# Optimization experiments

Hardware: AMD Instinct MI355X
Metric: run time of the kernel (lower is better)

The kernel has to match this reference:

```python
import jax, jax.numpy as jnp
import numpy as np


def setup_inputs() -> dict:
    key = jax.random.key(0)
    k1, k2 = jax.random.split(key)
    pred_corners = jax.random.normal(k1, (2048, 8, 3), dtype=jnp.float32)
    gt_corners = jax.random.normal(k2, (2048, 8, 3), dtype=jnp.float32)
    return {"pred_corners": pred_corners, "gt_corners": gt_corners}


def _chamfer(pred_corners, gt_corners):
    # flatten boxes -> point clouds: [Np*8, 3], [Ng*8, 3]
    x = pred_corners.reshape(-1, 3)
    y = gt_corners.reshape(-1, 3)
    x2 = jnp.sum(x * x, axis=-1)  # [N]
    y2 = jnp.sum(y * y, axis=-1)  # [M]
    d2 = x2[:, None] + y2[None, :] - 2.0 * jnp.einsum("nd,md->nm", x, y)
    dist = jnp.sqrt(jnp.maximum(d2, 0.0))  # [N, M]
    # bidirectional min, averaged per box (8 corners) then over boxes
    min_p2g = jnp.min(dist, axis=1).reshape(-1, 8).mean(axis=1)
    min_g2p = jnp.min(dist, axis=0).reshape(-1, 8).mean(axis=1)
    return min_p2g.mean() + min_g2p.mean()


def reference(pred_corners, gt_corners):
    return _chamfer(pred_corners, gt_corners)
```

## Files before the change

### kernel.cpp

```cpp
#include <hip/hip_runtime.h>


#define NPTS   16384
#define RPT    16
#define BLOCK  256
#define XPB    (RPT * BLOCK)
#define NXB    (NPTS / XPB)
#define NSEG   128
#define YSEG   (NPTS / NSEG)

__global__ __launch_bounds__(256) void init_mins(unsigned int* mins) {
    int i = blockIdx.x * blockDim.x + threadIdx.x;
    if (i < 2 * NPTS) mins[i] = 0x7F800000u;
}

__global__ __launch_bounds__(BLOCK, 4) void chamfer_min(
        const float* __restrict__ pred, const float* __restrict__ gt,
        unsigned int* __restrict__ mins) {
    const int xb  = blockIdx.x;
    const int ys  = blockIdx.y;
    const int dir = blockIdx.z;
    const float* __restrict__ X = dir ? gt : pred;
    const float* __restrict__ Y = dir ? pred : gt;
    unsigned int* __restrict__ outm = mins + dir * NPTS;
    const int tid = threadIdx.x;

    __shared__ float4 sh[YSEG];

    if (tid < YSEG) {
        int yi = ys * YSEG + tid;
        float a = Y[3 * yi + 0], b = Y[3 * yi + 1], c = Y[3 * yi + 2];
        sh[tid] = make_float4(a, b, c, -0.5f * (a * a + b * b + c * c));
    }

    float xx[RPT], xy[RPT], xz[RPT], x2[RPT], mx[RPT];
    const int xbase = xb * XPB;
#pragma unroll
    for (int r = 0; r < RPT; ++r) {
        int xi = xbase + r * BLOCK + tid;
        xx[r] = X[3 * xi + 0];
        xy[r] = X[3 * xi + 1];
        xz[r] = X[3 * xi + 2];
        x2[r] = xx[r] * xx[r] + xy[r] * xy[r] + xz[r] * xz[r];
        mx[r] = -3.0e38f;
    }

    __syncthreads();

#pragma unroll 2
    for (int j = 0; j < YSEG; ++j) {
        float4 y = sh[j];
#pragma unroll
        for (int r = 0; r < RPT; ++r) {
            float t = fmaf(xz[r], y.z, y.w);
            t = fmaf(xy[r], y.y, t);
            t = fmaf(xx[r], y.x, t);
            mx[r] = fmaxf(mx[r], t);
        }
    }

#pragma unroll
    for (int r = 0; r < RPT; ++r) {
        int xi = xbase + r * BLOCK + tid;
        float d2 = fmaxf(fmaf(-2.0f, mx[r], x2[r]), 0.0f);
        atomicMin(&outm[xi], __float_as_uint(d2));
    }
}

__global__ __launch_bounds__(1024) void chamfer_reduce(
        const unsigned int* __restrict__ mins, float* __restrict__ out) {
    const int tid = threadIdx.x;
    float s = 0.0f;
    for (int i = tid; i < 2 * NPTS; i += 1024)
        s += sqrtf(__uint_as_float(mins[i]));

#pragma unroll
    for (int off = 32; off > 0; off >>= 1)
        s += __shfl_down(s, off, 64);

    __shared__ float part[16];
    if ((tid & 63) == 0) part[tid >> 6] = s;
    __syncthreads();
    if (tid == 0) {
        float t = 0.0f;
#pragma unroll
        for (int w = 0; w < 16; ++w) t += part[w];
        out[0] = t / (float)NPTS;
    }
}

extern "C" void kernel_launch(void* const* d_in, const int* in_sizes, int n_in,
                              void* d_out, int out_size, void* d_ws, size_t ws_size,
                              hipStream_t stream) {
    const float* pred = (const float*)d_in[0];
    const float* gt   = (const float*)d_in[1];
    float* out        = (float*)d_out;
    unsigned int* mins = (unsigned int*)d_ws;

    hipLaunchKernelGGL(init_mins, dim3((2 * NPTS + 255) / 256), dim3(256), 0, stream,
                       mins);
    hipLaunchKernelGGL(chamfer_min, dim3(NXB, NSEG, 2), dim3(BLOCK), 0, stream,
                       pred, gt, mins);
    hipLaunchKernelGGL(chamfer_reduce, dim3(1), dim3(1024), 0, stream, mins, out);
}
```

Measured before the change: 107.2 us.

## Replace atomicMin with per-segment partial buffer and multi-block combine reduction

When the workspace is large enough, the main kernel writes each Y-segment's per-point max to a partial buffer instead of issuing atomicMin. A separate combine kernel takes the min over 64 segments, applies the sqrt and reduces per block, and a small final kernel sums the block results. This removes atomic contention and the single-block reduction, at the cost of an 8 MB partial buffer written and read back. Tile sizes also change (RPT 8, NSEG 64), the inner loop is unrolled by two Y points, and the fallback atomic path gets a multi-block reduction that uses atomicAdd.

```diff
diff --git a/kernel.cpp b/kernel.cpp
--- a/kernel.cpp
+++ b/kernel.cpp
@@ -2,19 +2,114 @@
 
 
 #define NPTS   16384
-#define RPT    16
+#define RPT    8
 #define BLOCK  256
 #define XPB    (RPT * BLOCK)
 #define NXB    (NPTS / XPB)
-#define NSEG   128
+#define NSEG   64
 #define YSEG   (NPTS / NSEG)
-
-__global__ __launch_bounds__(256) void init_mins(unsigned int* mins) {
+#define NPART  (2 * NSEG * NPTS)
+#define K2B    128
+#define WS_NEED ((NPART + K2B) * 4)
+
+
+__global__ __launch_bounds__(BLOCK, 4) void chamfer_partial(
+        const float* __restrict__ pred, const float* __restrict__ gt,
+        float* __restrict__ part) {
+    const int xb  = blockIdx.x;
+    const int ys  = blockIdx.y;
+    const int dir = blockIdx.z;
+    const float* __restrict__ X = dir ? gt : pred;
+    const float* __restrict__ Y = dir ? pred : gt;
+    const int tid = threadIdx.x;
+
+    __shared__ float4 sh[YSEG];
+    {
+        int yi = ys * YSEG + tid;
+        float a = Y[3 * yi + 0], b = Y[3 * yi + 1], c = Y[3 * yi + 2];
+        sh[tid] = make_float4(a, b, c, -0.5f * (a * a + b * b + c * c));
+    }
+
+    float xx[RPT], xy[RPT], xz[RPT], x2[RPT], mx[RPT];
+    const int xbase = xb * XPB;
+#pragma unroll
+    for (int r = 0; r < RPT; ++r) {
+        int xi = xbase + r * BLOCK + tid;
+        xx[r] = X[3 * xi + 0];
+        xy[r] = X[3 * xi + 1];
+        xz[r] = X[3 * xi + 2];
+        x2[r] = xx[r] * xx[r] + xy[r] * xy[r] + xz[r] * xz[r];
+        mx[r] = -3.0e38f;
+    }
+
+    __syncthreads();
+
+#pragma unroll 2
+    for (int j = 0; j < YSEG; j += 2) {
+        float4 y0 = sh[j];
+        float4 y1 = sh[j + 1];
+#pragma unroll
+        for (int r = 0; r < RPT; ++r) {
+            float t0 = fmaf(xz[r], y0.z, y0.w);
+            t0 = fmaf(xy[r], y0.y, t0);
+            t0 = fmaf(xx[r], y0.x, t0);
+            float t1 = fmaf(xz[r], y1.z, y1.w);
+            t1 = fmaf(xy[r], y1.y, t1);
+            t1 = fmaf(xx[r], y1.x, t1);
+            mx[r] = fmaxf(mx[r], fmaxf(t0, t1));
+        }
+    }
+
+    float* __restrict__ dst = part + (dir * NSEG + ys) * NPTS;
+#pragma unroll
+    for (int r = 0; r < RPT; ++r) {
+        int xi = xbase + r * BLOCK + tid;
+        dst[xi] = fmaf(-2.0f, mx[r], x2[r]);
+    }
+}
+
+__global__ __launch_bounds__(256) void chamfer_combine(
+        const float* __restrict__ part, float* __restrict__ sums) {
+    const int gid = blockIdx.x * 256 + threadIdx.x;
+    const int dir = gid >> 14;
+    const int x   = gid & (NPTS - 1);
+    float m = 3.0e38f;
+#pragma unroll 8
+    for (int s = 0; s < NSEG; ++s)
+        m = fminf(m, part[(dir * NSEG + s) * NPTS + x]);
+    float v = sqrtf(fmaxf(m, 0.0f));
+
+#pragma unroll
+    for (int off = 32; off > 0; off >>= 1)
+        v += __shfl_down(v, off, 64);
+
+    __shared__ float lsum[4];
+    if ((threadIdx.x & 63) == 0) lsum[threadIdx.x >> 6] = v;
+    __syncthreads();
+    if (threadIdx.x == 0)
+        sums[blockIdx.x] = lsum[0] + lsum[1] + lsum[2] + lsum[3];
+}
+
+__global__ __launch_bounds__(128) void chamfer_final(
+        const float* __restrict__ sums, float* __restrict__ out) {
+    float v = sums[threadIdx.x];
+#pragma unroll
+    for (int off = 32; off > 0; off >>= 1)
+        v += __shfl_down(v, off, 64);
+    __shared__ float w[2];
+    if ((threadIdx.x & 63) == 0) w[threadIdx.x >> 6] = v;
+    __syncthreads();
+    if (threadIdx.x == 0) out[0] = (w[0] + w[1]) * (1.0f / (float)NPTS);
+}
+
+
+__global__ __launch_bounds__(256) void init_mins(unsigned int* mins, float* out) {
     int i = blockIdx.x * blockDim.x + threadIdx.x;
     if (i < 2 * NPTS) mins[i] = 0x7F800000u;
-}
-
-__global__ __launch_bounds__(BLOCK, 4) void chamfer_min(
+    if (i == 0) out[0] = 0.0f;
+}
+
+__global__ __launch_bounds__(BLOCK, 4) void chamfer_min_atomic(
         const float* __restrict__ pred, const float* __restrict__ gt,
         unsigned int* __restrict__ mins) {
     const int xb  = blockIdx.x;
@@ -26,13 +121,11 @@
     const int tid = threadIdx.x;
 
     __shared__ float4 sh[YSEG];
-
-    if (tid < YSEG) {
+    {
         int yi = ys * YSEG + tid;
         float a = Y[3 * yi + 0], b = Y[3 * yi + 1], c = Y[3 * yi + 2];
         sh[tid] = make_float4(a, b, c, -0.5f * (a * a + b * b + c * c));
     }
-
     float xx[RPT], xy[RPT], xz[RPT], x2[RPT], mx[RPT];
     const int xbase = xb * XPB;
 #pragma unroll
@@ -44,21 +137,21 @@
         x2[r] = xx[r] * xx[r] + xy[r] * xy[r] + xz[r] * xz[r];
         mx[r] = -3.0e38f;
     }
-
-    __syncthreads();
-
+    __syncthreads();
 #pragma unroll 2
-    for (int j = 0; j < YSEG; ++j) {
-        float4 y = sh[j];
+    for (int j = 0; j < YSEG; j += 2) {
+        float4 y0 = sh[j], y1 = sh[j + 1];
 #pragma unroll
         for (int r = 0; r < RPT; ++r) {
-            float t = fmaf(xz[r], y.z, y.w);
-            t = fmaf(xy[r], y.y, t);
-            t = fmaf(xx[r], y.x, t);
-            mx[r] = fmaxf(mx[r], t);
+            float t0 = fmaf(xz[r], y0.z, y0.w);
+            t0 = fmaf(xy[r], y0.y, t0);
+            t0 = fmaf(xx[r], y0.x, t0);
+            float t1 = fmaf(xz[r], y1.z, y1.w);
+            t1 = fmaf(xy[r], y1.y, t1);
+            t1 = fmaf(xx[r], y1.x, t1);
+            mx[r] = fmaxf(mx[r], fmaxf(t0, t1));
         }
     }
-
 #pragma unroll
     for (int r = 0; r < RPT; ++r) {
         int xi = xbase + r * BLOCK + tid;
@@ -67,26 +160,18 @@
     }
 }
 
-__global__ __launch_bounds__(1024) void chamfer_reduce(
+__global__ __launch_bounds__(256) void chamfer_reduce_atomic(
         const unsigned int* __restrict__ mins, float* __restrict__ out) {
-    const int tid = threadIdx.x;
+    const int gid = blockIdx.x * 256 + threadIdx.x;
     float s = 0.0f;
-    for (int i = tid; i < 2 * NPTS; i += 1024)
-        s += sqrtf(__uint_as_float(mins[i]));
-
+#pragma unroll
+    for (int i = 0; i < 2; ++i)
+        s += sqrtf(__uint_as_float(mins[gid + i * 64 * 256]));
 #pragma unroll
     for (int off = 32; off > 0; off >>= 1)
         s += __shfl_down(s, off, 64);
-
-    __shared__ float part[16];
-    if ((tid & 63) == 0) part[tid >> 6] = s;
-    __syncthreads();
-    if (tid == 0) {
-        float t = 0.0f;
-#pragma unroll
-        for (int w = 0; w < 16; ++w) t += part[w];
-        out[0] = t / (float)NPTS;
-    }
+    if ((threadIdx.x & 63) == 0)
+        atomicAdd(out, s * (1.0f / (float)NPTS));
 }
 
 extern "C" void kernel_launch(void* const* d_in, const int* in_sizes, int n_in,
@@ -95,11 +180,23 @@
     const float* pred = (const float*)d_in[0];
     const float* gt   = (const float*)d_in[1];
     float* out        = (float*)d_out;
-    unsigned int* mins = (unsigned int*)d_ws;
-
-    hipLaunchKernelGGL(init_mins, dim3((2 * NPTS + 255) / 256), dim3(256), 0, stream,
-                       mins);
-    hipLaunchKernelGGL(chamfer_min, dim3(NXB, NSEG, 2), dim3(BLOCK), 0, stream,
-                       pred, gt, mins);
-    hipLaunchKernelGGL(chamfer_reduce, dim3(1), dim3(1024), 0, stream, mins, out);
-}
+
+    if (ws_size >= (size_t)WS_NEED) {
+        float* part = (float*)d_ws;
+        float* sums = part + NPART;
+        hipLaunchKernelGGL(chamfer_partial, dim3(NXB, NSEG, 2), dim3(BLOCK), 0,
+                           stream, pred, gt, part);
+        hipLaunchKernelGGL(chamfer_combine, dim3(K2B), dim3(256), 0, stream,
+                           part, sums);
+        hipLaunchKernelGGL(chamfer_final, dim3(1), dim3(128), 0, stream,
+                           sums, out);
+    } else {
+        unsigned int* mins = (unsigned int*)d_ws;
+        hipLaunchKernelGGL(init_mins, dim3((2 * NPTS + 255) / 256), dim3(256), 0,
+                           stream, mins, out);
+        hipLaunchKernelGGL(chamfer_min_atomic, dim3(NXB, NSEG, 2), dim3(BLOCK), 0,
+                           stream, pred, gt, mins);
+        hipLaunchKernelGGL(chamfer_reduce_atomic, dim3(64), dim3(256), 0, stream,
+                           mins, out);
+    }
+}
```

Result: slower. 110.0 us (+2.7%).
